# Kernel optimization log

Measured on AMD Instinct MI355X. Metric: run time of the kernel, lower is better.

Reference implementation:

```python
import jax, jax.numpy as jnp
import numpy as np

ALPHA = 1.5
N_ITER = 50


def entmax_bisect(X, alpha=ALPHA, n_iter=N_ITER):
    """entmax via 50-iteration bisection along axis 1 (Peters & Martins)."""
    d = X.shape[1]
    inv_am1 = 1.0 / (alpha - 1.0)

    def _p(Z):
        return jnp.clip(Z, 0.0) ** inv_am1

    Xs = X * (alpha - 1.0)
    max_val = Xs.max(axis=1, keepdims=True)                      # [B,1]
    tau_lo = max_val - 1.0                                       # gp(1) = 1
    tau_hi = max_val - (1.0 / d) ** (alpha - 1.0)                # gp(1/d)
    f_lo = _p(Xs - tau_lo).sum(axis=1, keepdims=True) - 1.0      # [B,1], fixed
    dm0 = tau_hi - tau_lo

    def body(carry, _):
        tau_lo, dm, _tau_m = carry
        dm = dm / 2.0
        tau_m = tau_lo + dm
        p_m = _p(Xs - tau_m)                                     # [B,d]
        f_m = p_m.sum(axis=1, keepdims=True) - 1.0
        tau_lo = jnp.where(f_m * f_lo >= 0, tau_m, tau_lo)
        return (tau_lo, dm, tau_m), None

    (tau_lo, dm, tau_m), _ = jax.lax.scan(
        body, (tau_lo, dm0, tau_lo), None, length=n_iter)
    p = _p(Xs - tau_m)                                           # last iterate
    # ensure_sum_one=True (entmax default)
    return p / p.sum(axis=1, keepdims=True)


def setup_inputs() -> dict:
    key = jax.random.key(0)
    k1, k2 = jax.random.split(key)
    B, V = 4096, 32000
    logits = jax.random.normal(k1, (B, V), dtype=jnp.float32)
    t = jax.random.uniform(k2, (B, V), dtype=jnp.float32)
    targets = t / t.sum(axis=1, keepdims=True)  # soft label distributions
    return {"logits": logits, "targets": targets}


def reference(logits, targets):
    alpha = ALPHA
    p = entmax_bisect(logits, alpha=alpha, n_iter=N_ITER)        # [B,V]
    omega = (1.0 - (p ** alpha).sum(axis=1)) / (alpha * (alpha - 1.0))
    return (omega + ((p - targets) * logits).sum(axis=1)).mean()
```

## Files before the change

kernel.cpp:

```cpp
#include <hip/hip_runtime.h>
#include <math.h>

constexpr int V_DIM  = 32000;
constexpr int NV4    = V_DIM / 4;
constexpr int TPB    = 1024;
constexpr int NCHUNK = (NV4 + TPB - 1) / TPB;
constexpr int CAP    = 8192;
constexpr int N_ITER = 50;

__global__ void zero_out_kernel(float* out) { out[0] = 0.0f; }

__global__ __launch_bounds__(TPB, 4) void entmax_loss_kernel(
    const float* __restrict__ X, const float* __restrict__ T,
    float* __restrict__ out, int B)
{
  const int row  = blockIdx.x;
  const float*  Xr = X + (size_t)row * V_DIM;
  const float4* X4 = (const float4*)Xr;
  const float4* T4 = (const float4*)(T + (size_t)row * V_DIM);
  const int tid  = threadIdx.x;
  const int lane = tid & 63;
  const int wid  = tid >> 6;

  __shared__ float s_wmax[16];
  __shared__ float s_wsum[16];
  __shared__ float s_res[2];
  __shared__ int   s_cnt;
  __shared__ float s_act[CAP];

  float4 xv[NCHUNK];
  float tmax = -INFINITY;
  float ttx  = 0.0f;
#pragma unroll
  for (int j = 0; j < NCHUNK; ++j) {
    const int idx = tid + j * TPB;
    if (idx < NV4) {
      const float4 x = X4[idx];
      const float4 t = T4[idx];
      xv[j] = x;
      tmax = fmaxf(tmax, fmaxf(fmaxf(x.x, x.y), fmaxf(x.z, x.w)));
      ttx += x.x * t.x;
      ttx += x.y * t.y;
      ttx += x.z * t.z;
      ttx += x.w * t.w;
    } else {
      xv[j] = make_float4(-INFINITY, -INFINITY, -INFINITY, -INFINITY);
    }
  }

#pragma unroll
  for (int o = 32; o >= 1; o >>= 1) {
    tmax = fmaxf(tmax, __shfl_xor(tmax, o));
    ttx += __shfl_xor(ttx, o);
  }
  if (lane == 0) { s_wmax[wid] = tmax; s_wsum[wid] = ttx; }
  if (tid == 0)  { s_cnt = 0; }
  __syncthreads();
  if (wid == 0) {
    float m = (lane < 16) ? s_wmax[lane] : -INFINITY;
    float s = (lane < 16) ? s_wsum[lane] : 0.0f;
#pragma unroll
    for (int o = 8; o >= 1; o >>= 1) {
      m = fmaxf(m, __shfl_xor(m, o));
      s += __shfl_xor(s, o);
    }
    if (lane == 0) { s_res[0] = m; s_res[1] = s; }
  }
  __syncthreads();

  const float maxX   = s_res[0];
  const float sum_tx = s_res[1];
  const float thr    = maxX - 2.0f;

#pragma unroll
  for (int j = 0; j < NCHUNK; ++j) {
    const int idx = tid + j * TPB;
    if (idx < NV4) {
      const float4 x = xv[j];
      if (x.x > thr) { int i = atomicAdd(&s_cnt, 1); if (i < CAP) s_act[i] = 0.5f * x.x; }
      if (x.y > thr) { int i = atomicAdd(&s_cnt, 1); if (i < CAP) s_act[i] = 0.5f * x.y; }
      if (x.z > thr) { int i = atomicAdd(&s_cnt, 1); if (i < CAP) s_act[i] = 0.5f * x.z; }
      if (x.w > thr) { int i = atomicAdd(&s_cnt, 1); if (i < CAP) s_act[i] = 0.5f * x.w; }
    }
  }
  __syncthreads();

  if (wid == 0) {
    const int  n_act   = s_cnt;
    const bool use_lds = (n_act <= CAP);
    const int  n       = use_lds ? n_act : V_DIM;

    const float maxXs  = 0.5f * maxX;
    const float tau_hi = maxXs - sqrtf(1.0f / (float)V_DIM);
    float tau_lo = maxXs - 1.0f;

    float s = 0.0f;
    for (int i = lane; i < n; i += 64) {
      const float xs = use_lds ? s_act[i] : 0.5f * Xr[i];
      const float r  = fmaxf(xs - tau_lo, 0.0f);
      s = fmaf(r, r, s);
    }
#pragma unroll
    for (int o = 32; o >= 1; o >>= 1) s += __shfl_xor(s, o);
    const float f_lo = s - 1.0f;

    float dm    = tau_hi - tau_lo;
    float tau_m = tau_lo;
    for (int it = 0; it < N_ITER; ++it) {
      dm *= 0.5f;
      tau_m = tau_lo + dm;
      float sm = 0.0f;
      for (int i = lane; i < n; i += 64) {
        const float xs = use_lds ? s_act[i] : 0.5f * Xr[i];
        const float r  = fmaxf(xs - tau_m, 0.0f);
        sm = fmaf(r, r, sm);
      }
#pragma unroll
      for (int o = 32; o >= 1; o >>= 1) sm += __shfl_xor(sm, o);
      const float f_m = sm - 1.0f;
      if (f_m * f_lo >= 0.0f) tau_lo = tau_m;
    }

    float S = 0.0f, Q3 = 0.0f, PX = 0.0f;
    for (int i = lane; i < n; i += 64) {
      const float xs = use_lds ? s_act[i] : 0.5f * Xr[i];
      const float r  = fmaxf(xs - tau_m, 0.0f);
      const float r2 = r * r;
      S  += r2;
      Q3 += r2 * r;
      PX += r2 * (2.0f * xs);
    }
#pragma unroll
    for (int o = 32; o >= 1; o >>= 1) {
      S  += __shfl_xor(S, o);
      Q3 += __shfl_xor(Q3, o);
      PX += __shfl_xor(PX, o);
    }
    if (lane == 0) {
      const float omega = (1.0f - Q3 / (S * sqrtf(S))) * (1.0f / 0.75f);
      const float loss  = omega + PX / S - sum_tx;
      atomicAdd(out, loss * (1.0f / (float)B));
    }
  }
}

extern "C" void kernel_launch(void* const* d_in, const int* in_sizes, int n_in,
                              void* d_out, int out_size, void* d_ws, size_t ws_size,
                              hipStream_t stream) {
  const float* logits  = (const float*)d_in[0];
  const float* targets = (const float*)d_in[1];
  float* out = (float*)d_out;
  const int B = in_sizes[0] / V_DIM;

  zero_out_kernel<<<1, 1, 0, stream>>>(out);
  entmax_loss_kernel<<<B, TPB, 0, stream>>>(logits, targets, out, B);
}
```

Measured before the change: 1.117 ms.

## Split row statistics and bisection into separate kernels with register-resident candidates

Splits the single-kernel design into two passes. The first is a row-stat kernel that computes max, the target dot product and the compacted candidate list, writing them to workspace. The second is a bisection kernel that runs one wave per row and holds the candidates in registers (8 or 32 per lane) for the 50 iterations. This removes the old pattern where one wave per 1024-thread block did the serial bisection while the other waves sat idle, which limited occupancy. The cost is an extra global round trip for candidates and a smaller LDS cap, with a fallback to the global row or the old kernel when the cap or workspace is exceeded.

```diff
diff --git a/kernel.cpp b/kernel.cpp
--- a/kernel.cpp
+++ b/kernel.cpp
@@ -3,51 +3,38 @@
 
 constexpr int V_DIM  = 32000;
 constexpr int NV4    = V_DIM / 4;
-constexpr int TPB    = 1024;
-constexpr int NCHUNK = (NV4 + TPB - 1) / TPB;
-constexpr int CAP    = 8192;
+constexpr int TPB_A  = 1024;
+constexpr int NCHUNK = (NV4 + TPB_A - 1) / TPB_A;
+constexpr int CAP    = 2048;
 constexpr int N_ITER = 50;
 
 __global__ void zero_out_kernel(float* out) { out[0] = 0.0f; }
 
-__global__ __launch_bounds__(TPB, 4) void entmax_loss_kernel(
+__global__ __launch_bounds__(TPB_A) void rowstat_kernel(
     const float* __restrict__ X, const float* __restrict__ T,
-    float* __restrict__ out, int B)
-{
-  const int row  = blockIdx.x;
-  const float*  Xr = X + (size_t)row * V_DIM;
-  const float4* X4 = (const float4*)Xr;
+    float* __restrict__ out, int* __restrict__ cnt_g,
+    float* __restrict__ maxs_g, float* __restrict__ act_g, float invB)
+{
+  const int row = blockIdx.x;
+  const float4* X4 = (const float4*)(X + (size_t)row * V_DIM);
   const float4* T4 = (const float4*)(T + (size_t)row * V_DIM);
-  const int tid  = threadIdx.x;
-  const int lane = tid & 63;
-  const int wid  = tid >> 6;
-
-  __shared__ float s_wmax[16];
-  __shared__ float s_wsum[16];
-  __shared__ float s_res[2];
+  const int tid = threadIdx.x, lane = tid & 63, wid = tid >> 6;
+
+  __shared__ float s_wmax[16], s_wsum[16], s_res[2];
   __shared__ int   s_cnt;
   __shared__ float s_act[CAP];
 
-  float4 xv[NCHUNK];
-  float tmax = -INFINITY;
-  float ttx  = 0.0f;
+  float tmax = -INFINITY, ttx = 0.0f;
 #pragma unroll
   for (int j = 0; j < NCHUNK; ++j) {
-    const int idx = tid + j * TPB;
+    const int idx = tid + j * TPB_A;
     if (idx < NV4) {
       const float4 x = X4[idx];
       const float4 t = T4[idx];
-      xv[j] = x;
       tmax = fmaxf(tmax, fmaxf(fmaxf(x.x, x.y), fmaxf(x.z, x.w)));
-      ttx += x.x * t.x;
-      ttx += x.y * t.y;
-      ttx += x.z * t.z;
-      ttx += x.w * t.w;
-    } else {
-      xv[j] = make_float4(-INFINITY, -INFINITY, -INFINITY, -INFINITY);
-    }
-  }
-
+      ttx = fmaf(x.x, t.x, fmaf(x.y, t.y, fmaf(x.z, t.z, fmaf(x.w, t.w, ttx))));
+    }
+  }
 #pragma unroll
   for (int o = 32; o >= 1; o >>= 1) {
     tmax = fmaxf(tmax, __shfl_xor(tmax, o));
@@ -68,15 +55,14 @@
   }
   __syncthreads();
 
-  const float maxX   = s_res[0];
-  const float sum_tx = s_res[1];
-  const float thr    = maxX - 2.0f;
+  const float maxX = s_res[0];
+  const float thr  = maxX - 2.0f;
 
 #pragma unroll
   for (int j = 0; j < NCHUNK; ++j) {
-    const int idx = tid + j * TPB;
+    const int idx = tid + j * TPB_A;
     if (idx < NV4) {
-      const float4 x = xv[j];
+      const float4 x = X4[idx];
       if (x.x > thr) { int i = atomicAdd(&s_cnt, 1); if (i < CAP) s_act[i] = 0.5f * x.x; }
       if (x.y > thr) { int i = atomicAdd(&s_cnt, 1); if (i < CAP) s_act[i] = 0.5f * x.y; }
       if (x.z > thr) { int i = atomicAdd(&s_cnt, 1); if (i < CAP) s_act[i] = 0.5f * x.z; }
@@ -85,61 +71,221 @@
   }
   __syncthreads();
 
+  const int cnt = s_cnt;
+  const int m   = min(cnt, CAP);
+  for (int i = tid; i < m; i += TPB_A) act_g[(size_t)row * CAP + i] = s_act[i];
+  if (tid == 0) {
+    cnt_g[row]  = cnt;
+    maxs_g[row] = 0.5f * maxX;
+    atomicAdd(out, -s_res[1] * invB);
+  }
+}
+
+template <int R>
+__device__ __forceinline__ float wave_row_loss(const float (&va)[R], float maxXs)
+{
+  const float tau_hi = maxXs - sqrtf(1.0f / (float)V_DIM);
+  float tau_lo = maxXs - 1.0f;
+
+  float s = 0.0f;
+#pragma unroll
+  for (int j = 0; j < R; ++j) { float r = fmaxf(va[j] - tau_lo, 0.0f); s = fmaf(r, r, s); }
+#pragma unroll
+  for (int o = 32; o >= 1; o >>= 1) s += __shfl_xor(s, o);
+  const float f_lo = s - 1.0f;
+
+  float dm = tau_hi - tau_lo, tau_m = tau_lo;
+  for (int it = 0; it < N_ITER; ++it) {
+    dm *= 0.5f;
+    tau_m = tau_lo + dm;
+    float sm = 0.0f;
+#pragma unroll
+    for (int j = 0; j < R; ++j) { float r = fmaxf(va[j] - tau_m, 0.0f); sm = fmaf(r, r, sm); }
+#pragma unroll
+    for (int o = 32; o >= 1; o >>= 1) sm += __shfl_xor(sm, o);
+    if ((sm - 1.0f) * f_lo >= 0.0f) tau_lo = tau_m;
+  }
+
+  float S = 0.0f, Q3 = 0.0f, PX = 0.0f;
+#pragma unroll
+  for (int j = 0; j < R; ++j) {
+    const float r = fmaxf(va[j] - tau_m, 0.0f);
+    const float r2 = r * r;
+    S += r2; Q3 += r2 * r; PX = fmaf(r2, 2.0f * va[j], PX);
+  }
+#pragma unroll
+  for (int o = 32; o >= 1; o >>= 1) {
+    S += __shfl_xor(S, o); Q3 += __shfl_xor(Q3, o); PX += __shfl_xor(PX, o);
+  }
+  return (1.0f - Q3 / (S * sqrtf(S))) * (1.0f / 0.75f) + PX / S;
+}
+
+__device__ float wave_row_loss_global(const float* __restrict__ Xr, float maxXs)
+{
+  const int lane = threadIdx.x & 63;
+  const float tau_hi = maxXs - sqrtf(1.0f / (float)V_DIM);
+  float tau_lo = maxXs - 1.0f;
+
+  float s = 0.0f;
+  for (int i = lane; i < V_DIM; i += 64) {
+    float r = fmaxf(0.5f * Xr[i] - tau_lo, 0.0f); s = fmaf(r, r, s);
+  }
+#pragma unroll
+  for (int o = 32; o >= 1; o >>= 1) s += __shfl_xor(s, o);
+  const float f_lo = s - 1.0f;
+
+  float dm = tau_hi - tau_lo, tau_m = tau_lo;
+  for (int it = 0; it < N_ITER; ++it) {
+    dm *= 0.5f; tau_m = tau_lo + dm;
+    float sm = 0.0f;
+    for (int i = lane; i < V_DIM; i += 64) {
+      float r = fmaxf(0.5f * Xr[i] - tau_m, 0.0f); sm = fmaf(r, r, sm);
+    }
+#pragma unroll
+    for (int o = 32; o >= 1; o >>= 1) sm += __shfl_xor(sm, o);
+    if ((sm - 1.0f) * f_lo >= 0.0f) tau_lo = tau_m;
+  }
+  float S = 0.0f, Q3 = 0.0f, PX = 0.0f;
+  for (int i = lane; i < V_DIM; i += 64) {
+    const float xs = 0.5f * Xr[i];
+    const float r = fmaxf(xs - tau_m, 0.0f);
+    const float r2 = r * r;
+    S += r2; Q3 += r2 * r; PX = fmaf(r2, 2.0f * xs, PX);
+  }
+#pragma unroll
+  for (int o = 32; o >= 1; o >>= 1) {
+    S += __shfl_xor(S, o); Q3 += __shfl_xor(Q3, o); PX += __shfl_xor(PX, o);
+  }
+  return (1.0f - Q3 / (S * sqrtf(S))) * (1.0f / 0.75f) + PX / S;
+}
+
+__global__ __launch_bounds__(256) void bisect_kernel(
+    const float* __restrict__ X, const int* __restrict__ cnt_g,
+    const float* __restrict__ maxs_g, const float* __restrict__ act_g,
+    float* __restrict__ out, int nrows, float invB)
+{
+  const int wid = threadIdx.x >> 6, lane = threadIdx.x & 63;
+  const int row = blockIdx.x * 4 + wid;
+  if (row >= nrows) return;
+  const int   n     = cnt_g[row];
+  const float maxXs = maxs_g[row];
+  const float* act  = act_g + (size_t)row * CAP;
+
+  float loss;
+  if (n <= 512) {
+    float va[8];
+#pragma unroll
+    for (int j = 0; j < 8; ++j) { int idx = j * 64 + lane; va[j] = (idx < n) ? act[idx] : -1e30f; }
+    loss = wave_row_loss<8>(va, maxXs);
+  } else if (n <= CAP) {
+    float va[32];
+#pragma unroll
+    for (int j = 0; j < 32; ++j) { int idx = j * 64 + lane; va[j] = (idx < n) ? act[idx] : -1e30f; }
+    loss = wave_row_loss<32>(va, maxXs);
+  } else {
+    loss = wave_row_loss_global(X + (size_t)row * V_DIM, maxXs);
+  }
+  if (lane == 0) atomicAdd(out, loss * invB);
+}
+
+__global__ __launch_bounds__(TPB_A) void entmax_loss_kernel(
+    const float* __restrict__ X, const float* __restrict__ T,
+    float* __restrict__ out, int B)
+{
+  const int row = blockIdx.x;
+  const float*  Xr = X + (size_t)row * V_DIM;
+  const float4* X4 = (const float4*)Xr;
+  const float4* T4 = (const float4*)(T + (size_t)row * V_DIM);
+  const int tid = threadIdx.x, lane = tid & 63, wid = tid >> 6;
+
+  __shared__ float s_wmax[16], s_wsum[16], s_res[2];
+  __shared__ int   s_cnt;
+  __shared__ float s_act[CAP];
+
+  float tmax = -INFINITY, ttx = 0.0f;
+#pragma unroll
+  for (int j = 0; j < NCHUNK; ++j) {
+    const int idx = tid + j * TPB_A;
+    if (idx < NV4) {
+      const float4 x = X4[idx], t = T4[idx];
+      tmax = fmaxf(tmax, fmaxf(fmaxf(x.x, x.y), fmaxf(x.z, x.w)));
+      ttx += x.x * t.x + x.y * t.y + x.z * t.z + x.w * t.w;
+    }
+  }
+#pragma unroll
+  for (int o = 32; o >= 1; o >>= 1) {
+    tmax = fmaxf(tmax, __shfl_xor(tmax, o));
+    ttx += __shfl_xor(ttx, o);
+  }
+  if (lane == 0) { s_wmax[wid] = tmax; s_wsum[wid] = ttx; }
+  if (tid == 0)  { s_cnt = 0; }
+  __syncthreads();
   if (wid == 0) {
-    const int  n_act   = s_cnt;
+    float m = (lane < 16) ? s_wmax[lane] : -INFINITY;
+    float s = (lane < 16) ? s_wsum[lane] : 0.0f;
+#pragma unroll
+    for (int o = 8; o >= 1; o >>= 1) { m = fmaxf(m, __shfl_xor(m, o)); s += __shfl_xor(s, o); }
+    if (lane == 0) { s_res[0] = m; s_res[1] = s; }
+  }
+  __syncthreads();
+
+  const float maxX = s_res[0], sum_tx = s_res[1], thr = maxX - 2.0f;
+#pragma unroll
+  for (int j = 0; j < NCHUNK; ++j) {
+    const int idx = tid + j * TPB_A;
+    if (idx < NV4) {
+      const float4 x = X4[idx];
+      if (x.x > thr) { int i = atomicAdd(&s_cnt, 1); if (i < CAP) s_act[i] = 0.5f * x.x; }
+      if (x.y > thr) { int i = atomicAdd(&s_cnt, 1); if (i < CAP) s_act[i] = 0.5f * x.y; }
+      if (x.z > thr) { int i = atomicAdd(&s_cnt, 1); if (i < CAP) s_act[i] = 0.5f * x.z; }
+      if (x.w > thr) { int i = atomicAdd(&s_cnt, 1); if (i < CAP) s_act[i] = 0.5f * x.w; }
+    }
+  }
+  __syncthreads();
+
+  if (wid == 0) {
+    const int  n_act = s_cnt;
     const bool use_lds = (n_act <= CAP);
-    const int  n       = use_lds ? n_act : V_DIM;
-
-    const float maxXs  = 0.5f * maxX;
+    const int  n = use_lds ? n_act : V_DIM;
+    const float maxXs = 0.5f * maxX;
     const float tau_hi = maxXs - sqrtf(1.0f / (float)V_DIM);
     float tau_lo = maxXs - 1.0f;
 
     float s = 0.0f;
     for (int i = lane; i < n; i += 64) {
       const float xs = use_lds ? s_act[i] : 0.5f * Xr[i];
-      const float r  = fmaxf(xs - tau_lo, 0.0f);
-      s = fmaf(r, r, s);
+      const float r = fmaxf(xs - tau_lo, 0.0f); s = fmaf(r, r, s);
     }
 #pragma unroll
     for (int o = 32; o >= 1; o >>= 1) s += __shfl_xor(s, o);
     const float f_lo = s - 1.0f;
 
-    float dm    = tau_hi - tau_lo;
-    float tau_m = tau_lo;
+    float dm = tau_hi - tau_lo, tau_m = tau_lo;
     for (int it = 0; it < N_ITER; ++it) {
-      dm *= 0.5f;
-      tau_m = tau_lo + dm;
+      dm *= 0.5f; tau_m = tau_lo + dm;
       float sm = 0.0f;
       for (int i = lane; i < n; i += 64) {
         const float xs = use_lds ? s_act[i] : 0.5f * Xr[i];
-        const float r  = fmaxf(xs - tau_m, 0.0f);
-        sm = fmaf(r, r, sm);
+        const float r = fmaxf(xs - tau_m, 0.0f); sm = fmaf(r, r, sm);
       }
 #pragma unroll
       for (int o = 32; o >= 1; o >>= 1) sm += __shfl_xor(sm, o);
-      const float f_m = sm - 1.0f;
-      if (f_m * f_lo >= 0.0f) tau_lo = tau_m;
-    }
-
+      if ((sm - 1.0f) * f_lo >= 0.0f) tau_lo = tau_m;
+    }
     float S = 0.0f, Q3 = 0.0f, PX = 0.0f;
     for (int i = lane; i < n; i += 64) {
       const float xs = use_lds ? s_act[i] : 0.5f * Xr[i];
-      const float r  = fmaxf(xs - tau_m, 0.0f);
+      const float r = fmaxf(xs - tau_m, 0.0f);
       const float r2 = r * r;
-      S  += r2;
-      Q3 += r2 * r;
-      PX += r2 * (2.0f * xs);
+      S += r2; Q3 += r2 * r; PX += r2 * (2.0f * xs);
     }
 #pragma unroll
     for (int o = 32; o >= 1; o >>= 1) {
-      S  += __shfl_xor(S, o);
-      Q3 += __shfl_xor(Q3, o);
-      PX += __shfl_xor(PX, o);
+      S += __shfl_xor(S, o); Q3 += __shfl_xor(Q3, o); PX += __shfl_xor(PX, o);
     }
     if (lane == 0) {
       const float omega = (1.0f - Q3 / (S * sqrtf(S))) * (1.0f / 0.75f);
-      const float loss  = omega + PX / S - sum_tx;
-      atomicAdd(out, loss * (1.0f / (float)B));
+      atomicAdd(out, (omega + PX / S - sum_tx) * (1.0f / (float)B));
     }
   }
 }
@@ -147,11 +293,22 @@
 extern "C" void kernel_launch(void* const* d_in, const int* in_sizes, int n_in,
                               void* d_out, int out_size, void* d_ws, size_t ws_size,
                               hipStream_t stream) {
-  const float* logits  = (const float*)d_in[0];
-  const float* targets = (const float*)d_in[1];
+  const float* X = (const float*)d_in[0];
+  const float* T = (const float*)d_in[1];
   float* out = (float*)d_out;
-  const int B = in_sizes[0] / V_DIM;
+  const int rows = in_sizes[0] / V_DIM;
+  const float invB = 1.0f / (float)rows;
 
   zero_out_kernel<<<1, 1, 0, stream>>>(out);
-  entmax_loss_kernel<<<B, TPB, 0, stream>>>(logits, targets, out, B);
-}
+
+  const size_t need = (size_t)rows * 8 + (size_t)rows * CAP * 4;
+  if (ws_size >= need) {
+    int*   cnt_g  = (int*)d_ws;
+    float* maxs_g = (float*)((char*)d_ws + (size_t)rows * 4);
+    float* act_g  = (float*)((char*)d_ws + (size_t)rows * 8);
+    rowstat_kernel<<<rows, TPB_A, 0, stream>>>(X, T, out, cnt_g, maxs_g, act_g, invB);
+    bisect_kernel<<<(rows + 3) / 4, 256, 0, stream>>>(X, cnt_g, maxs_g, act_g, out, rows, invB);
+  } else {
+    entmax_loss_kernel<<<rows, TPB_A, 0, stream>>>(X, T, out, rows);
+  }
+}
```

Result: slower. 3.681 ms (+229.6%).
